# Kernel tuning notes

Hardware: AMD Instinct MI355X
Metric: run time of the kernel (lower is better)

The kernel has to match this reference:

```python
import jax, jax.numpy as jnp
import numpy as np

B, S, D_IN, D_OUT = 8, 2048, 1024, 1024


def setup_inputs() -> dict:
    key = jax.random.key(0)
    ks = jax.random.split(key, 9)
    sc = 1.0 / np.sqrt(D_IN)
    return {
        "in_k": jax.random.normal(ks[0], (B, S, D_IN), jnp.float32),
        "in_q": jax.random.normal(ks[1], (B, S, D_IN), jnp.float32),
        "in_v": jax.random.normal(ks[2], (B, S, D_IN), jnp.float32),
        "Wk": jax.random.normal(ks[3], (D_IN, D_OUT), jnp.float32) * sc,
        "bk": jax.random.normal(ks[4], (D_OUT,), jnp.float32) * sc,
        "Wq": jax.random.normal(ks[5], (D_IN, D_OUT), jnp.float32) * sc,
        "bq": jax.random.normal(ks[6], (D_OUT,), jnp.float32) * sc,
        "Wv": jax.random.normal(ks[7], (D_IN, D_OUT), jnp.float32) * sc,
        "bv": jax.random.normal(ks[8], (D_OUT,), jnp.float32) * sc,
    }


def reference(in_k, in_q, in_v, Wk, bk, Wq, bq, Wv, bv):
    k = in_k @ Wk + bk  # [B,S,D]
    q = in_q @ Wq + bq
    v = in_v @ Wv + bv
    scale = 1.0 / jnp.sqrt(jnp.asarray(D_OUT, q.dtype))
    scores = jnp.einsum("bqd,bkd->bqk", q, k) * scale  # [B,S,S]
    attn = jax.nn.softmax(scores, axis=-1)
    return jnp.einsum("bqk,bkd->bqd", attn, v)
```

## Files before the change

kernel.cpp:

```cpp
#include <hip/hip_runtime.h>
#include <hip/hip_bf16.h>
#include <stdint.h>

typedef __bf16 bf16x8 __attribute__((ext_vector_type(8)));
typedef float  f32x4  __attribute__((ext_vector_type(4)));
typedef uint16_t u16x8 __attribute__((ext_vector_type(8)));

__device__ __forceinline__ uint16_t f32_to_bf16(float f) {
    union { float f; uint32_t u; } v; v.f = f;
    uint32_t u = v.u;
    uint32_t r = (u + 0x7FFFu + ((u >> 16) & 1u)) >> 16;
    return (uint16_t)r;
}

__device__ __forceinline__ void gld16(const void* g, void* l) {
    __builtin_amdgcn_global_load_lds(
        (const __attribute__((address_space(1))) void*)g,
        (__attribute__((address_space(3))) void*)l,
        16, 0, 0);
}

#define MFMA16 __builtin_amdgcn_mfma_f32_16x16x32_bf16
#define SBAR   __builtin_amdgcn_s_barrier
#define SCHED0() __builtin_amdgcn_sched_barrier(0)
#define PRIO   __builtin_amdgcn_s_setprio
#define VMC2()   asm volatile("s_waitcnt vmcnt(2)" ::: "memory")
#define VMCNT0() asm volatile("s_waitcnt vmcnt(0)" ::: "memory")
#define LGKM4()  asm volatile("s_waitcnt lgkmcnt(4)" ::: "memory")
#define LGKM8()  asm volatile("s_waitcnt lgkmcnt(8)" ::: "memory")
#define KEEP(x)  asm volatile("" :: "v"(*(const float*)&(x)))

__global__ __launch_bounds__(256) void cast3_kernel(
    const float* __restrict__ i0, const float* __restrict__ i1,
    const float* __restrict__ i2, uint16_t* __restrict__ o0,
    uint16_t* __restrict__ o1, uint16_t* __restrict__ o2) {
    const float* in = (blockIdx.z == 0) ? i0 : (blockIdx.z == 1) ? i1 : i2;
    uint16_t* out = (blockIdx.z == 0) ? o0 : (blockIdx.z == 1) ? o1 : o2;
    size_t i = ((size_t)blockIdx.x * 256 + threadIdx.x) * 8;
    float4 a = *(const float4*)(in + i);
    float4 b = *(const float4*)(in + i + 4);
    u16x8 o;
    o[0] = f32_to_bf16(a.x); o[1] = f32_to_bf16(a.y);
    o[2] = f32_to_bf16(a.z); o[3] = f32_to_bf16(a.w);
    o[4] = f32_to_bf16(b.x); o[5] = f32_to_bf16(b.y);
    o[6] = f32_to_bf16(b.z); o[7] = f32_to_bf16(b.w);
    *(u16x8*)(out + i) = o;
}

__global__ __launch_bounds__(256) void wtrans_kernel(
    const float* __restrict__ W0, const float* __restrict__ W1,
    const float* __restrict__ W2, uint16_t* __restrict__ Wt0) {
    const float* W = (blockIdx.z == 0) ? W0 : (blockIdx.z == 1) ? W1 : W2;
    uint16_t* Wt = Wt0 + (size_t)blockIdx.z * 1024 * 1024;
    __shared__ float tile[64][65];
    const int n0 = blockIdx.x * 64, k0 = blockIdx.y * 64;
    const int tx = threadIdx.x & 63, ty0 = threadIdx.x >> 6;
#pragma unroll
    for (int r = 0; r < 16; ++r) {
        int ty = ty0 + r * 4;
        tile[ty][tx] = W[(size_t)(k0 + ty) * 1024 + n0 + tx];
    }
    __syncthreads();
#pragma unroll
    for (int r = 0; r < 16; ++r) {
        int ty = ty0 + r * 4;
        Wt[(size_t)(n0 + ty) * 1024 + k0 + tx] = f32_to_bf16(tile[tx][ty]);
    }
}

__device__ __forceinline__ void stageA64(const uint16_t* __restrict__ G, int ldg,
                                         int k0, int rowbase, uint16_t* ldsT, int tid) {
    const int l = tid >> 3;
    const int ch = tid & 7;
    const int c = ((ch ^ (l & 7)) << 3);
    gld16(G + (size_t)(rowbase + l) * ldg + k0 + c,
          ldsT + (size_t)(rowbase + l) * 64 + ch * 8);
}

__device__ __forceinline__ void stageB64(const uint16_t* __restrict__ G, int ldg,
                                         int k0, int h, int j, uint16_t* ldsT, int tid) {
    const int lloc = j * 64 + (tid >> 3);
    const int ch = tid & 7;
    const int grow = (lloc & 31) + ((lloc >> 5) << 6) + (h << 5);
    const int c = ((ch ^ (lloc & 7)) << 3);
    gld16(G + (size_t)grow * ldg + k0 + c,
          ldsT + (size_t)(h * 128 + lloc) * 64 + ch * 8);
}

__device__ __forceinline__ void rdA(bf16x8 (&dst)[4][2], const uint16_t* s,
                                    int abase, int mb, int c0, int c1) {
#pragma unroll
    for (int m = 0; m < 4; ++m) {
        dst[m][0] = *(const bf16x8*)&s[abase + (mb + m) * 1024 + c0];
        dst[m][1] = *(const bf16x8*)&s[abase + (mb + m) * 1024 + c1];
    }
}

__device__ __forceinline__ void rdB(bf16x8 (&dst)[2][2], const uint16_t* s,
                                    int bb, int h, int c0, int c1) {
#pragma unroll
    for (int n = 0; n < 2; ++n) {
        dst[n][0] = *(const bf16x8*)&s[bb + h * 8192 + n * 1024 + c0];
        dst[n][1] = *(const bf16x8*)&s[bb + h * 8192 + n * 1024 + c1];
    }
}

__device__ __forceinline__ void mm8(f32x4 (&acc)[8][4], int mb, int nh,
                                    const bf16x8 (&a)[4][2], const bf16x8 (&b)[2][2]) {
#pragma unroll
    for (int m = 0; m < 4; ++m)
#pragma unroll
        for (int n = 0; n < 2; ++n) {
            acc[mb + m][nh * 2 + n] =
                MFMA16(a[m][0], b[n][0], acc[mb + m][nh * 2 + n], 0, 0, 0);
            acc[mb + m][nh * 2 + n] =
                MFMA16(a[m][1], b[n][1], acc[mb + m][nh * 2 + n], 0, 0, 0);
        }
}

__device__ __forceinline__ void gemm_core(const uint16_t* __restrict__ A, int lda,
                                          const uint16_t* __restrict__ B, int ldb,
                                          int K, f32x4 (&acc)[8][4]) {
    __shared__ __align__(16) uint16_t As[2][16384];
    __shared__ __align__(16) uint16_t Bs[2][16384];
    const int tid  = threadIdx.x;
    const int lane = tid & 63;
    const int wave = tid >> 6;
    const int wr = wave >> 2, wcn = wave & 3;
    const int mrow = lane & 15, q = lane >> 4;
    const int sx = mrow & 7;
    const int c0 = ((q ^ sx) << 3);
    const int c1 = (((4 + q) ^ sx) << 3);
    const int abase = (wr * 128 + mrow) * 64;
    const int bb    = (wcn * 32 + mrow) * 64;

    uint16_t* As0 = As[0]; uint16_t* As1 = As[1];
    uint16_t* Bs0 = Bs[0]; uint16_t* Bs1 = Bs[1];

    bf16x8 Xa[4][2], Ya[4][2], Xb[2][2], Yb[2][2];

    stageA64(A, lda, 0, 0,   As0, tid); stageA64(A, lda, 0, 128, As0, tid);
    stageB64(B, ldb, 0, 0, 0, Bs0, tid); stageB64(B, ldb, 0, 0, 1, Bs0, tid);
    stageB64(B, ldb, 0, 1, 0, Bs0, tid); stageB64(B, ldb, 0, 1, 1, Bs0, tid);
    stageA64(A, lda, 0, 64,  As0, tid); stageA64(A, lda, 0, 192, As0, tid);
    VMCNT0();
    __syncthreads();
    rdA(Xa, As0, abase, 0, c0, c1);
    rdB(Xb, Bs0, bb, 0, c0, c1);

    const int NT = K >> 6;
    for (int it = 0; it < NT; it += 2) {
        const int k1 = (it + 1) << 6;
        const int k2 = (it + 2 < NT) ? ((it + 2) << 6) : 0;

        rdB(Yb, Bs0, bb, 1, c0, c1);
        stageA64(A, lda, k1, 0, As1, tid); stageA64(A, lda, k1, 128, As1, tid);
        VMC2(); SBAR(); LGKM4(); SCHED0();
        PRIO(1); mm8(acc, 0, 0, Xa, Xb); PRIO(0); SBAR(); SCHED0();

        rdA(Ya, As0, abase, 4, c0, c1);
        stageB64(B, ldb, k1, 0, 0, Bs1, tid); stageB64(B, ldb, k1, 0, 1, Bs1, tid);
        VMC2(); SBAR(); LGKM8(); SCHED0();
        PRIO(1); mm8(acc, 0, 1, Xa, Yb); PRIO(0); SBAR(); SCHED0();

        rdA(Xa, As1, abase, 0, c0, c1);
        stageB64(B, ldb, k1, 1, 0, Bs1, tid); stageB64(B, ldb, k1, 1, 1, Bs1, tid);
        VMC2(); SBAR(); LGKM8(); SCHED0();
        PRIO(1); mm8(acc, 4, 1, Ya, Yb); PRIO(0); SBAR(); SCHED0();

        rdB(Yb, Bs1, bb, 0, c0, c1);
        stageA64(A, lda, k1, 64, As1, tid); stageA64(A, lda, k1, 192, As1, tid);
        VMC2(); SBAR(); LGKM4(); SCHED0();
        PRIO(1); mm8(acc, 4, 0, Ya, Xb); PRIO(0); SBAR(); SCHED0();

        rdB(Xb, Bs1, bb, 1, c0, c1);
        stageA64(A, lda, k2, 0, As0, tid); stageA64(A, lda, k2, 128, As0, tid);
        VMC2(); SBAR(); LGKM4(); SCHED0();
        PRIO(1); mm8(acc, 0, 0, Xa, Yb); PRIO(0); SBAR(); SCHED0();

        rdA(Ya, As1, abase, 4, c0, c1);
        stageB64(B, ldb, k2, 0, 0, Bs0, tid); stageB64(B, ldb, k2, 0, 1, Bs0, tid);
        VMC2(); SBAR(); LGKM8(); SCHED0();
        PRIO(1); mm8(acc, 0, 1, Xa, Xb); PRIO(0); SBAR(); SCHED0();

        rdA(Xa, As0, abase, 0, c0, c1);
        stageB64(B, ldb, k2, 1, 0, Bs0, tid); stageB64(B, ldb, k2, 1, 1, Bs0, tid);
        VMC2(); SBAR(); LGKM8(); SCHED0();
        PRIO(1); mm8(acc, 4, 1, Ya, Xb); PRIO(0); SBAR(); SCHED0();

        rdB(Xb, Bs0, bb, 0, c0, c1);
        stageA64(A, lda, k2, 64, As0, tid); stageA64(A, lda, k2, 192, As0, tid);
        VMC2(); SBAR(); LGKM4(); SCHED0();
        PRIO(1); mm8(acc, 4, 0, Ya, Yb); PRIO(0); SBAR(); SCHED0();
    }
    VMCNT0();
    KEEP(Xa[0][0]); KEEP(Xa[0][1]); KEEP(Xa[1][0]); KEEP(Xa[1][1]);
    KEEP(Xa[2][0]); KEEP(Xa[2][1]); KEEP(Xa[3][0]); KEEP(Xa[3][1]);
    KEEP(Xb[0][0]); KEEP(Xb[0][1]); KEEP(Xb[1][0]); KEEP(Xb[1][1]);
}

__global__ __launch_bounds__(512, 2) void proj256_kernel(
    const uint16_t* __restrict__ Ab, const uint16_t* __restrict__ Bb,
    uint16_t* __restrict__ Cb, uint16_t* __restrict__ Vt,
    const float* __restrict__ b0, const float* __restrict__ b1,
    const float* __restrict__ b2) {
    const int bid = blockIdx.x;
    const int lg = (bid & 7) * 96 + (bid >> 3);
    const int pidx = lg >> 8;
    const int t = lg & 255;
    const int band = t >> 4;
    const int Mt = band * 4 + (t & 3);
    const int Nt = (t >> 2) & 3;
    const int row0 = Mt * 256, col0 = Nt * 256;

    const uint16_t* A = Ab + (size_t)pidx * 16777216 + (size_t)row0 * 1024;
    const uint16_t* B = Bb + (size_t)pidx * 1048576 + (size_t)col0 * 1024;
    const float* bias = (pidx == 0) ? b0 : (pidx == 1) ? b1 : b2;

    f32x4 acc[8][4];
#pragma unroll
    for (int i = 0; i < 8; ++i)
#pragma unroll
        for (int j = 0; j < 4; ++j) acc[i][j] = 0.0f;

    gemm_core(A, 1024, B, 1024, 1024, acc);

    const int tid = threadIdx.x, lane = tid & 63, wave = tid >> 6;
    const int wr = wave >> 2, wcn = wave & 3;
    const int mrow = lane & 15, quad = lane >> 4;
    float bv_[4];
#pragma unroll
    for (int n = 0; n < 4; ++n) bv_[n] = bias[col0 + wcn * 64 + n * 16 + mrow];

    if (pidx < 2) {
        uint16_t* C = Cb + (size_t)pidx * 16777216;
#pragma unroll
        for (int m = 0; m < 8; ++m)
#pragma unroll
            for (int n = 0; n < 4; ++n)
#pragma unroll
                for (int r = 0; r < 4; ++r) {
                    int row = row0 + wr * 128 + m * 16 + quad * 4 + r;
                    int col = col0 + wcn * 64 + n * 16 + mrow;
                    C[(size_t)row * 1024 + col] = f32_to_bf16(acc[m][n][r] + bv_[n]);
                }
    } else {
#pragma unroll
        for (int m = 0; m < 8; ++m)
#pragma unroll
            for (int n = 0; n < 4; ++n)
#pragma unroll
                for (int r = 0; r < 4; ++r) {
                    int row = row0 + wr * 128 + m * 16 + quad * 4 + r;
                    int col = col0 + wcn * 64 + n * 16 + mrow;
                    Vt[((size_t)(row >> 11) * 1024 + col) * 2048 + (row & 2047)] =
                        f32_to_bf16(acc[m][n][r] + bv_[n]);
                }
    }
}

template <int EPI>
__global__ __launch_bounds__(512, 2) void att256_kernel(
    const uint16_t* __restrict__ Abase, int lda, long long sAz,
    const uint16_t* __restrict__ Bbase, int ldb, long long sBz,
    void* __restrict__ Cv, int ldc, long long sCz,
    int K, float alpha, float* __restrict__ sums, int NtN, int chunk) {
    const int bid = blockIdx.x;
    const int lg = (bid & 7) * chunk + (bid >> 3);
    const int z = lg / chunk;
    const int t = lg % chunk;
    const int r2 = t & (2 * NtN - 1);
    const int band = t / (2 * NtN);
    const int Mt = band * 2 + (r2 & 1);
    const int Nt = r2 >> 1;
    const int row0 = Mt * 256, col0 = Nt * 256;

    const uint16_t* A = Abase + (size_t)z * sAz + (size_t)row0 * lda;
    const uint16_t* B = Bbase + (size_t)z * sBz + (size_t)col0 * ldb;

    f32x4 acc[8][4];
#pragma unroll
    for (int i = 0; i < 8; ++i)
#pragma unroll
        for (int j = 0; j < 4; ++j) acc[i][j] = 0.0f;

    gemm_core(A, lda, B, ldb, K, acc);

    const int tid = threadIdx.x, lane = tid & 63, wave = tid >> 6;
    const int wr = wave >> 2, wcn = wave & 3;
    const int mrow = lane & 15, quad = lane >> 4;

    if (EPI == 1) {
        uint16_t* C = (uint16_t*)Cv + (size_t)z * sCz;
#pragma unroll
        for (int m = 0; m < 8; ++m)
#pragma unroll
            for (int r = 0; r < 4; ++r) {
                int row = row0 + wr * 128 + m * 16 + quad * 4 + r;
                float s = 0.0f;
#pragma unroll
                for (int n = 0; n < 4; ++n) {
                    int col = col0 + wcn * 64 + n * 16 + mrow;
                    float e = __expf(acc[m][n][r] * alpha);
                    C[(size_t)row * ldc + col] = f32_to_bf16(e);
                    s += e;
                }
                s += __shfl_xor(s, 1, 64);
                s += __shfl_xor(s, 2, 64);
                s += __shfl_xor(s, 4, 64);
                s += __shfl_xor(s, 8, 64);
                if (mrow == 0) atomicAdd(&sums[(size_t)z * 2048 + row], s);
            }
    } else {
        float* C = (float*)Cv + (size_t)z * sCz;
#pragma unroll
        for (int m = 0; m < 8; ++m)
#pragma unroll
            for (int r = 0; r < 4; ++r) {
                int row = row0 + wr * 128 + m * 16 + quad * 4 + r;
                float inv = 1.0f / sums[(size_t)z * 2048 + row];
#pragma unroll
                for (int n = 0; n < 4; ++n) {
                    int col = col0 + wcn * 64 + n * 16 + mrow;
                    C[(size_t)row * ldc + col] = acc[m][n][r] * inv;
                }
            }
    }
}

extern "C" void kernel_launch(void* const* d_in, const int* in_sizes, int n_in,
                              void* d_out, int out_size, void* d_ws, size_t ws_size,
                              hipStream_t stream) {
    const float* in_k = (const float*)d_in[0];
    const float* in_q = (const float*)d_in[1];
    const float* in_v = (const float*)d_in[2];
    const float* Wk = (const float*)d_in[3];
    const float* bk = (const float*)d_in[4];
    const float* Wq = (const float*)d_in[5];
    const float* bq = (const float*)d_in[6];
    const float* Wv = (const float*)d_in[7];
    const float* bv = (const float*)d_in[8];
    float* out = (float*)d_out;

    char* w = (char*)d_ws;
    uint16_t* Xq  = (uint16_t*)(w + 0);
    uint16_t* Xk  = (uint16_t*)(w + 33554432);
    uint16_t* Xv  = (uint16_t*)(w + 67108864);
    uint16_t* Qb  = (uint16_t*)(w + 100663296);
    uint16_t* Kb  = (uint16_t*)(w + 134217728);
    uint16_t* Vt  = (uint16_t*)(w + 167772160);
    uint16_t* Wqt = (uint16_t*)(w + 201326592);
    uint16_t* Sc  = Xq;
    float*    sums = (float*)Xv;

    wtrans_kernel<<<dim3(16, 16, 3), 256, 0, stream>>>(Wq, Wk, Wv, Wqt);
    cast3_kernel<<<dim3(8192, 1, 3), 256, 0, stream>>>(in_q, in_k, in_v, Xq, Xk, Xv);

    proj256_kernel<<<768, 512, 0, stream>>>(Xq, Wqt, Qb, Vt, bq, bk, bv);

    hipMemsetAsync(sums, 0, 8 * 2048 * sizeof(float), stream);

    att256_kernel<1><<<512, 512, 0, stream>>>(
        Qb, 1024, 2048LL * 1024, Kb, 1024, 2048LL * 1024,
        Sc, 2048, 2048LL * 2048, 1024, 0.03125f, sums, 8, 64);

    att256_kernel<2><<<256, 512, 0, stream>>>(
        Sc, 2048, 2048LL * 2048, Vt, 2048, 1024LL * 2048,
        out, 1024, 2048LL * 1024, 2048, 1.0f, sums, 4, 32);
}
```

Baseline: 609.2 us.

## Restructure projection GEMM pipeline to prefetch two K-tiles ahead with fewer register fragments

Rewrites the LDS double-buffered main loop of the projection GEMM. It now preloads two K-tiles in the prologue, allows six outstanding global loads instead of two, and reads A/B fragments from LDS just before each MFMA phase. The old scheme held X/Y register pairs across phases. The change frees registers and deepens the global-load lookahead, at the cost of waiting on full LDS reads (lgkmcnt 0) before each MFMA cluster. That wait may expose LDS latency. Writing into buffers while other waves still read them also depends on the barrier placement being correct.

```diff
diff --git a/kernel.cpp b/kernel.cpp
--- a/kernel.cpp
+++ b/kernel.cpp
@@ -24,11 +24,10 @@
 #define SBAR   __builtin_amdgcn_s_barrier
 #define SCHED0() __builtin_amdgcn_sched_barrier(0)
 #define PRIO   __builtin_amdgcn_s_setprio
-#define VMC2()   asm volatile("s_waitcnt vmcnt(2)" ::: "memory")
+#define VMC6()   asm volatile("s_waitcnt vmcnt(6)" ::: "memory")
 #define VMCNT0() asm volatile("s_waitcnt vmcnt(0)" ::: "memory")
-#define LGKM4()  asm volatile("s_waitcnt lgkmcnt(4)" ::: "memory")
+#define LGKM0()  asm volatile("s_waitcnt lgkmcnt(0)" ::: "memory")
 #define LGKM8()  asm volatile("s_waitcnt lgkmcnt(8)" ::: "memory")
-#define KEEP(x)  asm volatile("" :: "v"(*(const float*)&(x)))
 
 __global__ __launch_bounds__(256) void cast3_kernel(
     const float* __restrict__ i0, const float* __restrict__ i1,
@@ -121,8 +120,10 @@
 __device__ __forceinline__ void gemm_core(const uint16_t* __restrict__ A, int lda,
                                           const uint16_t* __restrict__ B, int ldb,
                                           int K, f32x4 (&acc)[8][4]) {
-    __shared__ __align__(16) uint16_t As[2][16384];
-    __shared__ __align__(16) uint16_t Bs[2][16384];
+    __shared__ __align__(16) uint16_t AsBuf[2][16384];
+    __shared__ __align__(16) uint16_t BsBuf[2][16384];
+    uint16_t* As0 = AsBuf[0]; uint16_t* As1 = AsBuf[1];
+    uint16_t* Bs0 = BsBuf[0]; uint16_t* Bs1 = BsBuf[1];
     const int tid  = threadIdx.x;
     const int lane = tid & 63;
     const int wave = tid >> 6;
@@ -134,69 +135,67 @@
     const int abase = (wr * 128 + mrow) * 64;
     const int bb    = (wcn * 32 + mrow) * 64;
 
-    uint16_t* As0 = As[0]; uint16_t* As1 = As[1];
-    uint16_t* Bs0 = Bs[0]; uint16_t* Bs1 = Bs[1];
-
-    bf16x8 Xa[4][2], Ya[4][2], Xb[2][2], Yb[2][2];
+    const int NT = K >> 6;
 
     stageA64(A, lda, 0, 0,   As0, tid); stageA64(A, lda, 0, 128, As0, tid);
     stageB64(B, ldb, 0, 0, 0, Bs0, tid); stageB64(B, ldb, 0, 0, 1, Bs0, tid);
     stageB64(B, ldb, 0, 1, 0, Bs0, tid); stageB64(B, ldb, 0, 1, 1, Bs0, tid);
     stageA64(A, lda, 0, 64,  As0, tid); stageA64(A, lda, 0, 192, As0, tid);
+    stageA64(A, lda, 64, 0,   As1, tid); stageA64(A, lda, 64, 128, As1, tid);
+    stageB64(B, ldb, 64, 0, 0, Bs1, tid); stageB64(B, ldb, 64, 0, 1, Bs1, tid);
+    stageB64(B, ldb, 64, 1, 0, Bs1, tid); stageB64(B, ldb, 64, 1, 1, Bs1, tid);
+    VMC6();
+    __syncthreads();
+
+    bf16x8 af[4][2], bA[2][2], bB[2][2];
+    for (int t = 0; t < NT; t += 2) {
+        const int k1 = (t + 1) << 6;
+        const int k2 = (t + 2 < NT) ? ((t + 2) << 6) : 0;
+        const int k3 = (t + 3 < NT) ? ((t + 3) << 6) : 0;
+
+        stageA64(A, lda, k1, 64, As1, tid); stageA64(A, lda, k1, 192, As1, tid);
+        rdA(af, As0, abase, 0, c0, c1);
+        rdB(bA, Bs0, bb, 0, c0, c1);
+        LGKM8(); SBAR(); LGKM0(); SCHED0();
+        PRIO(1); mm8(acc, 0, 0, af, bA); PRIO(0); SBAR(); SCHED0();
+
+        stageA64(A, lda, k2, 0, As0, tid); stageA64(A, lda, k2, 128, As0, tid);
+        rdB(bB, Bs0, bb, 1, c0, c1);
+        SBAR(); LGKM0(); SCHED0();
+        PRIO(1); mm8(acc, 0, 1, af, bB); PRIO(0); SBAR(); SCHED0();
+
+        stageB64(B, ldb, k2, 0, 0, Bs0, tid); stageB64(B, ldb, k2, 0, 1, Bs0, tid);
+        rdA(af, As0, abase, 4, c0, c1);
+        SBAR(); LGKM0(); SCHED0();
+        PRIO(1); mm8(acc, 4, 1, af, bB); PRIO(0); SBAR(); SCHED0();
+
+        stageB64(B, ldb, k2, 1, 0, Bs0, tid); stageB64(B, ldb, k2, 1, 1, Bs0, tid);
+        SBAR(); SCHED0();
+        PRIO(1); mm8(acc, 4, 0, af, bA); PRIO(0);
+        VMC6(); SBAR(); SCHED0();
+
+        stageA64(A, lda, k2, 64, As0, tid); stageA64(A, lda, k2, 192, As0, tid);
+        rdA(af, As1, abase, 0, c0, c1);
+        rdB(bA, Bs1, bb, 0, c0, c1);
+        LGKM8(); SBAR(); LGKM0(); SCHED0();
+        PRIO(1); mm8(acc, 0, 0, af, bA); PRIO(0); SBAR(); SCHED0();
+
+        stageA64(A, lda, k3, 0, As1, tid); stageA64(A, lda, k3, 128, As1, tid);
+        rdB(bB, Bs1, bb, 1, c0, c1);
+        SBAR(); LGKM0(); SCHED0();
+        PRIO(1); mm8(acc, 0, 1, af, bB); PRIO(0); SBAR(); SCHED0();
+
+        stageB64(B, ldb, k3, 0, 0, Bs1, tid); stageB64(B, ldb, k3, 0, 1, Bs1, tid);
+        rdA(af, As1, abase, 4, c0, c1);
+        SBAR(); LGKM0(); SCHED0();
+        PRIO(1); mm8(acc, 4, 1, af, bB); PRIO(0); SBAR(); SCHED0();
+
+        stageB64(B, ldb, k3, 1, 0, Bs1, tid); stageB64(B, ldb, k3, 1, 1, Bs1, tid);
+        SBAR(); SCHED0();
+        PRIO(1); mm8(acc, 4, 0, af, bA); PRIO(0);
+        VMC6(); SBAR(); SCHED0();
+    }
     VMCNT0();
-    __syncthreads();
-    rdA(Xa, As0, abase, 0, c0, c1);
-    rdB(Xb, Bs0, bb, 0, c0, c1);
-
-    const int NT = K >> 6;
-    for (int it = 0; it < NT; it += 2) {
-        const int k1 = (it + 1) << 6;
-        const int k2 = (it + 2 < NT) ? ((it + 2) << 6) : 0;
-
-        rdB(Yb, Bs0, bb, 1, c0, c1);
-        stageA64(A, lda, k1, 0, As1, tid); stageA64(A, lda, k1, 128, As1, tid);
-        VMC2(); SBAR(); LGKM4(); SCHED0();
-        PRIO(1); mm8(acc, 0, 0, Xa, Xb); PRIO(0); SBAR(); SCHED0();
-
-        rdA(Ya, As0, abase, 4, c0, c1);
-        stageB64(B, ldb, k1, 0, 0, Bs1, tid); stageB64(B, ldb, k1, 0, 1, Bs1, tid);
-        VMC2(); SBAR(); LGKM8(); SCHED0();
-        PRIO(1); mm8(acc, 0, 1, Xa, Yb); PRIO(0); SBAR(); SCHED0();
-
-        rdA(Xa, As1, abase, 0, c0, c1);
-        stageB64(B, ldb, k1, 1, 0, Bs1, tid); stageB64(B, ldb, k1, 1, 1, Bs1, tid);
-        VMC2(); SBAR(); LGKM8(); SCHED0();
-        PRIO(1); mm8(acc, 4, 1, Ya, Yb); PRIO(0); SBAR(); SCHED0();
-
-        rdB(Yb, Bs1, bb, 0, c0, c1);
-        stageA64(A, lda, k1, 64, As1, tid); stageA64(A, lda, k1, 192, As1, tid);
-        VMC2(); SBAR(); LGKM4(); SCHED0();
-        PRIO(1); mm8(acc, 4, 0, Ya, Xb); PRIO(0); SBAR(); SCHED0();
-
-        rdB(Xb, Bs1, bb, 1, c0, c1);
-        stageA64(A, lda, k2, 0, As0, tid); stageA64(A, lda, k2, 128, As0, tid);
-        VMC2(); SBAR(); LGKM4(); SCHED0();
-        PRIO(1); mm8(acc, 0, 0, Xa, Yb); PRIO(0); SBAR(); SCHED0();
-
-        rdA(Ya, As1, abase, 4, c0, c1);
-        stageB64(B, ldb, k2, 0, 0, Bs0, tid); stageB64(B, ldb, k2, 0, 1, Bs0, tid);
-        VMC2(); SBAR(); LGKM8(); SCHED0();
-        PRIO(1); mm8(acc, 0, 1, Xa, Xb); PRIO(0); SBAR(); SCHED0();
-
-        rdA(Xa, As0, abase, 0, c0, c1);
-        stageB64(B, ldb, k2, 1, 0, Bs0, tid); stageB64(B, ldb, k2, 1, 1, Bs0, tid);
-        VMC2(); SBAR(); LGKM8(); SCHED0();
-        PRIO(1); mm8(acc, 4, 1, Ya, Xb); PRIO(0); SBAR(); SCHED0();
-
-        rdB(Xb, Bs0, bb, 0, c0, c1);
-        stageA64(A, lda, k2, 64, As0, tid); stageA64(A, lda, k2, 192, As0, tid);
-        VMC2(); SBAR(); LGKM4(); SCHED0();
-        PRIO(1); mm8(acc, 4, 0, Ya, Yb); PRIO(0); SBAR(); SCHED0();
-    }
-    VMCNT0();
-    KEEP(Xa[0][0]); KEEP(Xa[0][1]); KEEP(Xa[1][0]); KEEP(Xa[1][1]);
-    KEEP(Xa[2][0]); KEEP(Xa[2][1]); KEEP(Xa[3][0]); KEEP(Xa[3][1]);
-    KEEP(Xb[0][0]); KEEP(Xb[0][1]); KEEP(Xb[1][0]); KEEP(Xb[1][1]);
 }
 
 __global__ __launch_bounds__(512, 2) void proj256_kernel(
```

Measured after the change: 555.1 us. -8.9%, faster.
